# Kernel tuning notes

Measured on AMD Instinct MI355X. Metric: run time of the kernel, lower is better.

The kernel has to match this reference:

```python
import jax, jax.numpy as jnp
import numpy as np

# Mamba3TextEncoder config (class .small() defaults)
B_SZ, SEQ = 4, 512
VOCAB, D_MODEL, N_LAYERS = 32000, 768, 12
N_STATE, EXPAND, HEADDIM, NGROUPS, EMBED = 64, 2, 32, 1, 1536
D_INNER = EXPAND * D_MODEL            # 1536
NHEADS = D_INNER // HEADDIM           # 48
CONV_DIM = D_INNER + 2 * NGROUPS * N_STATE  # 1664 (x, B, C go through depthwise conv)
K_CONV = 4
PROJ_IN = 2 * D_INNER + 2 * NGROUPS * N_STATE + NHEADS  # z, xBC, dt


def setup_inputs() -> dict:
    key = jax.random.key(0)
    ks = jax.random.split(key, 16)
    s = 0.02
    return {
        "token_ids": jax.random.randint(ks[0], (B_SZ, SEQ), 0, VOCAB),
        "embed_W": jax.random.normal(ks[1], (VOCAB, D_MODEL), jnp.float32) * s,
        "ln_W": jnp.ones((N_LAYERS, D_MODEL), jnp.float32),
        "in_proj_W": jax.random.normal(ks[2], (N_LAYERS, D_MODEL, PROJ_IN), jnp.float32) * s,
        "conv_W": jax.random.normal(ks[3], (N_LAYERS, CONV_DIM, 1, K_CONV), jnp.float32) * 0.1,
        "conv_b": jnp.zeros((N_LAYERS, CONV_DIM), jnp.float32),
        "dt_bias": jax.random.uniform(ks[4], (N_LAYERS, NHEADS), jnp.float32, -4.6, -2.0),
        "A_log": jnp.tile(jnp.log(jnp.arange(1, NHEADS + 1, dtype=jnp.float32))[None], (N_LAYERS, 1)),
        "D": jnp.ones((N_LAYERS, NHEADS), jnp.float32),
        "norm_W": jnp.ones((N_LAYERS, D_INNER), jnp.float32),
        "out_proj_W": jax.random.normal(ks[5], (N_LAYERS, D_INNER, D_MODEL), jnp.float32) * s,
        "final_norm_W": jnp.ones((D_MODEL,), jnp.float32),
        "proj_W": jax.random.normal(ks[6], (D_MODEL, EMBED), jnp.float32) * s,
        "proj_b": jnp.zeros((EMBED,), jnp.float32),
    }


def _rmsnorm(x, w, eps=1e-5):
    return x * jax.lax.rsqrt(jnp.mean(x * x, axis=-1, keepdims=True) + eps) * w


def _causal_conv(x, w, b):
    # x: [B,S,C] depthwise causal conv, kernel K_CONV
    y = jax.lax.conv_general_dilated(
        x.transpose(0, 2, 1), w, (1,), [(K_CONV - 1, 0)],
        dimension_numbers=("NCH", "OIH", "NCH"), feature_group_count=CONV_DIM)
    return y.transpose(0, 2, 1) + b


def _ssm(xs, dt, A, Bm, Cm):
    # selective scan. xs:[B,S,H,P] dt:[B,S,H] A:[H] Bm,Cm:[B,S,N] (ngroups=1)
    decay = jnp.exp(dt * A)              # [B,S,H]
    dtx = dt[..., None] * xs             # [B,S,H,P]
    h0 = jnp.zeros((xs.shape[0], NHEADS, HEADDIM, N_STATE), xs.dtype)

    def step(h, inp):
        dec, dx, b, c = inp              # [B,H],[B,H,P],[B,N],[B,N]
        h = dec[..., None, None] * h + dx[..., None] * b[:, None, None, :]
        y = jnp.einsum("bhpn,bn->bhp", h, c)
        return h, y

    inputs = (decay.transpose(1, 0, 2), dtx.transpose(1, 0, 2, 3),
              Bm.transpose(1, 0, 2), Cm.transpose(1, 0, 2))
    _, ys = jax.lax.scan(step, h0, inputs)
    return ys.transpose(1, 0, 2, 3)      # [B,S,H,P]


def reference(token_ids, embed_W, ln_W, in_proj_W, conv_W, conv_b, dt_bias,
              A_log, D, norm_W, out_proj_W, final_norm_W, proj_W, proj_b):
    x = embed_W[token_ids]                               # [B,S,D]
    for l in range(N_LAYERS):
        h = _rmsnorm(x, ln_W[l])
        zxbcdt = h @ in_proj_W[l]                        # [B,S,PROJ_IN]
        z = zxbcdt[..., :D_INNER]
        xBC = zxbcdt[..., D_INNER:D_INNER + CONV_DIM]
        dt_raw = zxbcdt[..., D_INNER + CONV_DIM:]        # [B,S,H]
        xBC = jax.nn.silu(_causal_conv(xBC, conv_W[l], conv_b[l]))
        xs = xBC[..., :D_INNER].reshape(*xBC.shape[:2], NHEADS, HEADDIM)
        Bm = xBC[..., D_INNER:D_INNER + N_STATE]
        Cm = xBC[..., D_INNER + N_STATE:]
        dt = jax.nn.softplus(dt_raw + dt_bias[l])
        A = -jnp.exp(A_log[l])
        y = _ssm(xs, dt, A, Bm, Cm) + D[l][None, None, :, None] * xs
        y = y.reshape(*y.shape[:2], D_INNER)
        y = _rmsnorm(y * jax.nn.silu(z), norm_W[l])      # gated RMSNorm
        x = x + y @ out_proj_W[l]
    x = _rmsnorm(x, final_norm_W)
    pooled = x.mean(axis=1)                              # [B,D]
    proj = pooled @ proj_W + proj_b                      # [B,EMBED]
    n = jnp.sqrt(jnp.sum(proj * proj, axis=-1, keepdims=True))
    return proj / jnp.maximum(n, 1e-12)
```

## Files before the change

### kernel.cpp

```cpp
#include <hip/hip_runtime.h>
#include <math.h>

typedef __bf16 bf16x8 __attribute__((ext_vector_type(8)));
typedef short  s16x8  __attribute__((ext_vector_type(8)));
typedef float  f32x4  __attribute__((ext_vector_type(4)));

static constexpr int BSZ = 4, SEQ = 512, DM = 768;
static constexpr int DIN = 1536, NH = 48, HP = 32, NS = 64;
static constexpr int CDIM = 1664;
static constexpr int PROJ_IN = 3248;
static constexpr int LDZX = 3328;
static constexpr int ROWS = BSZ * SEQ;
static constexpr int EMBED = 1536;
static constexpr int NLAYERS = 12;

using gptr_t = const __attribute__((address_space(1))) void*;
using lptr_t = __attribute__((address_space(3))) void*;

__device__ __forceinline__ unsigned short f2bf(float f) {
  unsigned u = __builtin_bit_cast(unsigned, f);
  u += 0x7FFF + ((u >> 16) & 1);
  return (unsigned short)(u >> 16);
}
__device__ __forceinline__ float bf2f(unsigned short u) {
  unsigned v = (unsigned)u << 16;
  return __builtin_bit_cast(float, v);
}
__device__ __forceinline__ float sigm(float x) { return 1.f / (1.f + __expf(-x)); }
__device__ __forceinline__ float sp(float x) { return (x > 15.f) ? x : log1pf(__expf(x)); }

__device__ __forceinline__ void gll16(const void* g, void* l) {
  __builtin_amdgcn_global_load_lds((gptr_t)g, (lptr_t)l, 16, 0, 0);
}
__device__ __forceinline__ f32x4 mfma16(s16x8 a, s16x8 b, f32x4 c) {
  return __builtin_amdgcn_mfma_f32_16x16x32_bf16(
      __builtin_bit_cast(bf16x8, a), __builtin_bit_cast(bf16x8, b), c, 0, 0, 0);
}

template <int NW>
__device__ __forceinline__ float block_sum(float v) {
#pragma unroll
  for (int o = 32; o; o >>= 1) v += __shfl_xor(v, o);
  __shared__ float red[NW];
  if ((threadIdx.x & 63) == 0) red[threadIdx.x >> 6] = v;
  __syncthreads();
  float s = red[0];
#pragma unroll
  for (int i = 1; i < NW; ++i) s += red[i];
  return s;
}

__global__ void embed_k(const int* __restrict__ tok, const float* __restrict__ eW,
                        float* __restrict__ x, unsigned short* __restrict__ x16,
                        float* __restrict__ ssq1p) {
  int bt = blockIdx.x, tid = threadIdx.x;
  float4 v = ((const float4*)(eW + (size_t)tok[bt] * DM))[tid];
  ((float4*)(x + (size_t)bt * DM))[tid] = v;
  unsigned long long pk =
      (unsigned long long)f2bf(v.x) | ((unsigned long long)f2bf(v.y) << 16) |
      ((unsigned long long)f2bf(v.z) << 32) | ((unsigned long long)f2bf(v.w) << 48);
  *(unsigned long long*)(x16 + (size_t)bt * DM + tid * 4) = pk;
  float ss = v.x * v.x + v.y * v.y + v.z * v.z + v.w * v.w;
  float tot = block_sum<3>(ss);
  if (tid < 24) ssq1p[(size_t)bt * 24 + tid] = (tid == 0) ? tot : 0.f;
}

__global__ void transpose_cvt(const float* __restrict__ W, const float* __restrict__ sc,
                              unsigned short* __restrict__ Wt, int K, int N, int Npad) {
  __shared__ float tile[32][33];
  int l = blockIdx.z;
  const float* Wl = W + (size_t)l * K * N;
  const float* scl = sc + (size_t)l * K;
  unsigned short* Wtl = Wt + (size_t)l * Npad * K;
  int nb = blockIdx.x * 32, kb = blockIdx.y * 32;
  int tx = threadIdx.x, ty = threadIdx.y;
#pragma unroll
  for (int r = 0; r < 4; ++r) {
    int k = kb + ty + r * 8, n = nb + tx;
    tile[ty + r * 8][tx] = (n < N) ? Wl[(size_t)k * N + n] * scl[k] : 0.f;
  }
  __syncthreads();
#pragma unroll
  for (int r = 0; r < 4; ++r) {
    int n = nb + ty + r * 8, k = kb + tx;
    Wtl[(size_t)n * K + k] = f2bf(tile[tx][ty + r * 8]);
  }
}

template <int BM, int BN, int MODE>
__global__ __launch_bounds__(256) void gemm_k(
    const unsigned short* __restrict__ A, const unsigned short* __restrict__ Bt,
    int K, const float* __restrict__ ssqp, void* __restrict__ O0,
    void* __restrict__ O1, void* __restrict__ O2,
    unsigned short* __restrict__ x16o, float* __restrict__ ssqo) {
  constexpr int AIT = BM / 32, BIT = BN / 32, NST = AIT + BIT;
  constexpr int FM = BM / 32, FN = BN / 32;
  constexpr int NSSQ = (MODE == 0) ? 24 : 48;
  constexpr float INVD = (MODE == 0) ? (1.f / 768.f) : (1.f / 1536.f);
  __shared__ unsigned short lA[2][BM * 64], lB[2][BN * 64];
  __shared__ float rss[BM];
  int tid = threadIdx.x, lane = tid & 63, wv = tid >> 6;
  int flat = blockIdx.y * gridDim.x + blockIdx.x;
  int q8 = (gridDim.x * gridDim.y) >> 3;
  int nf = (flat & 7) * q8 + (flat >> 3);
  int bx = nf % gridDim.x, by = nf / gridDim.x;
  int m0 = by * BM, n0 = bx * BN;
  int wm = (wv >> 1) * (BM / 2), wn = (wv & 1) * (BN / 2);
  int NK = K >> 6;
  auto stage = [&](int kt, int buf) {
#pragma unroll
    for (int i = 0; i < AIT; ++i) {
      int flt = i * 256 + tid, rr = flt >> 3, cc = flt & 7;
      gll16(A + (size_t)(m0 + rr) * K + kt + (cc ^ (rr & 7)) * 8, (char*)lA[buf] + flt * 16);
    }
#pragma unroll
    for (int i = 0; i < BIT; ++i) {
      int flt = i * 256 + tid, rr = flt >> 3, cc = flt & 7;
      gll16(Bt + (size_t)(n0 + rr) * K + kt + (cc ^ (rr & 7)) * 8, (char*)lB[buf] + flt * 16);
    }
  };
  stage(0, 0);
  if (tid < BM) {
    const float* p = ssqp + (size_t)(m0 + tid) * NSSQ;
    float s = 0.f;
#pragma unroll
    for (int j = 0; j < NSSQ; ++j) s += p[j];
    rss[tid] = rsqrtf(s * INVD + 1e-5f);
  }
  __syncthreads();
  f32x4 acc[FM][FN] = {};
  for (int i = 0; i < NK; ++i) {
    if (i + 1 < NK) {
      stage((i + 1) << 6, (i + 1) & 1);
      asm volatile("s_waitcnt vmcnt(%0)" :: "i"(NST) : "memory");
    } else {
      asm volatile("s_waitcnt vmcnt(0)" ::: "memory");
    }
    __builtin_amdgcn_s_barrier();
    __builtin_amdgcn_sched_barrier(0);
    const unsigned short* cA = lA[i & 1];
    const unsigned short* cB = lB[i & 1];
#pragma unroll
    for (int ks = 0; ks < 2; ++ks) {
      s16x8 a[FM], b[FN];
#pragma unroll
      for (int mi = 0; mi < FM; ++mi) {
        int row = wm + mi * 16 + (lane & 15);
        int ch = (ks * 4 + (lane >> 4)) ^ (row & 7);
        a[mi] = *(const s16x8*)((const char*)cA + row * 128 + ch * 16);
      }
#pragma unroll
      for (int nj = 0; nj < FN; ++nj) {
        int row = wn + nj * 16 + (lane & 15);
        int ch = (ks * 4 + (lane >> 4)) ^ (row & 7);
        b[nj] = *(const s16x8*)((const char*)cB + row * 128 + ch * 16);
      }
#pragma unroll
      for (int mi = 0; mi < FM; ++mi)
#pragma unroll
        for (int nj = 0; nj < FN; ++nj)
          acc[mi][nj] = mfma16(a[mi], b[nj], acc[mi][nj]);
    }
    __builtin_amdgcn_s_barrier();
  }
#pragma unroll
  for (int mi = 0; mi < FM; ++mi) {
    int rl0 = wm + mi * 16 + ((lane >> 4) << 2);
    float rsr[4];
#pragma unroll
    for (int rg = 0; rg < 4; ++rg) rsr[rg] = rss[rl0 + rg];
    float part[4] = {0.f, 0.f, 0.f, 0.f};
#pragma unroll
    for (int nj = 0; nj < FN; ++nj) {
      int col = n0 + wn + nj * 16 + (lane & 15);
#pragma unroll
      for (int rg = 0; rg < 4; ++rg) {
        int row = m0 + rl0 + rg;
        float vv = acc[mi][nj][rg] * rsr[rg];
        if constexpr (MODE == 0) {
          if (n0 < DIN) {
            ((unsigned short*)O0)[(size_t)row * DIN + col] = f2bf(vv);
          } else if (n0 < DIN + CDIM) {
            ((float*)O1)[(size_t)row * CDIM + (col - DIN)] = vv;
          } else {
            int c2 = col - (DIN + CDIM);
            if (c2 < NH) ((float*)O2)[(size_t)row * NH + c2] = vv;
          }
        } else {
          size_t idx = (size_t)row * DM + col;
          float xn = vv + ((float*)O0)[idx];
          ((float*)O0)[idx] = xn;
          x16o[idx] = f2bf(xn);
          part[rg] += xn * xn;
        }
      }
    }
    if constexpr (MODE == 1) {
#pragma unroll
      for (int rg = 0; rg < 4; ++rg) {
#pragma unroll
        for (int off = 1; off < 16; off <<= 1) part[rg] += __shfl_xor(part[rg], off);
      }
      if ((lane & 15) == 0) {
#pragma unroll
        for (int rg = 0; rg < 4; ++rg)
          ssqo[(size_t)(m0 + rl0 + rg) * 24 + bx * 2 + (wn >> 5)] = part[rg];
      }
    }
  }
}

__global__ __launch_bounds__(256) void conv_dt_k(
    const float* __restrict__ xbc, const float* __restrict__ cw, const float* __restrict__ cb,
    const float* __restrict__ dtraw, const float* __restrict__ dbias,
    unsigned short* __restrict__ xs16, unsigned short* __restrict__ dtxT,
    unsigned short* __restrict__ Bbf, unsigned short* __restrict__ Cbf,
    float* __restrict__ dts) {
  __shared__ float stg[11][256];
  __shared__ float dtl[8][48];
  int tid = threadIdx.x;
  int chunk = blockIdx.x;
  int bt0 = blockIdx.y * 8;
  int t0 = bt0 & (SEQ - 1);
  int cbase = chunk * 256;
#pragma unroll
  for (int i = 0; i < 11; ++i) {
    int s = t0 - 3 + i, col = cbase + tid;
    stg[i][tid] = (s >= 0 && col < CDIM) ? xbc[(size_t)(bt0 - 3 + i) * CDIM + col] : 0.f;
  }
  if (chunk < 6) {
    for (int idx = tid; idx < 384; idx += 256) {
      int r = idx / 48, hh = idx - r * 48;
      dtl[r][hh] = sp(dtraw[(size_t)(bt0 + r) * NH + hh] + dbias[hh]);
    }
  }
  __syncthreads();
  int c = cbase + tid;
  if (chunk < 6) {
    float w0 = cw[c * 4], w1 = cw[c * 4 + 1], w2 = cw[c * 4 + 2], w3 = cw[c * 4 + 3];
    float bias = cb[c];
    int hh = c >> 5, p = c & 31, b = bt0 >> 9;
    s16x8 pk;
#pragma unroll
    for (int r = 0; r < 8; ++r) {
      float a = bias + stg[r][tid] * w0 + stg[r + 1][tid] * w1 + stg[r + 2][tid] * w2 +
                stg[r + 3][tid] * w3;
      float sv = a * sigm(a);
      xs16[(size_t)(bt0 + r) * DIN + c] = f2bf(sv);
      pk[r] = (short)f2bf(sv * dtl[r][hh]);
    }
    *reinterpret_cast<s16x8*>(dtxT + ((((size_t)b * NH + hh) * HP + p) * SEQ + t0)) = pk;
  } else if (tid < 128) {
    int cc = DIN + tid;
    float w0 = cw[cc * 4], w1 = cw[cc * 4 + 1], w2 = cw[cc * 4 + 2], w3 = cw[cc * 4 + 3];
    float bias = cb[cc];
#pragma unroll
    for (int r = 0; r < 8; ++r) {
      float a = bias + stg[r][tid] * w0 + stg[r + 1][tid] * w1 + stg[r + 2][tid] * w2 +
                stg[r + 3][tid] * w3;
      float sv = a * sigm(a);
      if (tid < 64) Bbf[(size_t)(bt0 + r) * NS + tid] = f2bf(sv);
      else          Cbf[(size_t)(bt0 + r) * NS + (tid - 64)] = f2bf(sv);
    }
  } else if (tid < 176) {
    int hh = tid - 128;
    float bias_ = dbias[hh];
    float v[8];
#pragma unroll
    for (int r = 0; r < 8; ++r) v[r] = sp(dtraw[(size_t)(bt0 + r) * NH + hh] + bias_);
    float4 a4 = {v[0], v[1], v[2], v[3]}, b4 = {v[4], v[5], v[6], v[7]};
    float* dp = dts + ((size_t)(bt0 >> 9) * NH + hh) * SEQ + t0;
    *(float4*)dp = a4;
    *(float4*)(dp + 4) = b4;
  }
}

__global__ __launch_bounds__(256) void scan_k(
    const unsigned short* __restrict__ Bbf, const unsigned short* __restrict__ Cbf,
    const unsigned short* __restrict__ dtxT, const unsigned short* __restrict__ xs16,
    const float* __restrict__ dts, const unsigned short* __restrict__ zb,
    const float* __restrict__ alog, const float* __restrict__ Dvec,
    unsigned short* __restrict__ g16, float* __restrict__ ssq2p) {
  __shared__ unsigned short CbPt[64 * 64];
  __shared__ unsigned short Bb[2][64 * 64], Dx[2][32 * 64];
  __shared__ float lsb[SEQ];
  __shared__ float pair[256];
  __shared__ int sfirst;
  int tid = threadIdx.x, lane = tid & 63, wv = tid >> 6;
  int tb = blockIdx.x, h = blockIdx.y, b = blockIdx.z;
  int t0 = tb * 64;
  const unsigned short* dxrow = dtxT + ((size_t)b * NH + h) * HP * SEQ;

#pragma unroll
  for (int i = 0; i < 2; ++i) {
    int flt = i * 256 + tid, rr = flt >> 3, cc = flt & 7;
    gll16(Cbf + (size_t)(b * SEQ + t0 + rr) * NS + (cc ^ (rr & 7)) * 8, (char*)CbPt + flt * 16);
  }
  float Ah = -__expf(alog[h]);
  int t2 = tid * 2;
  float2 dv = *(const float2*)(dts + ((size_t)b * NH + h) * SEQ + t2);
  float d0 = dv.x * Ah, d1 = dv.y * Ah;
  pair[tid] = d0 + d1;
  __syncthreads();
  for (int off = 1; off < 256; off <<= 1) {
    float add = (tid >= off) ? pair[tid - off] : 0.f;
    float cur = pair[tid];
    __syncthreads();
    pair[tid] = cur + add;
    __syncthreads();
  }
  float excl = tid ? pair[tid - 1] : 0.f;
  lsb[t2] = excl + d0;
  lsb[t2 + 1] = excl + d0 + d1;
  if (tid == 0) sfirst = tb;
  __syncthreads();
  float REF = lsb[t0];
  if (tid < tb && (REF - lsb[tid * 64 + 63] >= -12.f)) atomicMin(&sfirst, tid);
  __syncthreads();
  int st0 = sfirst;

#pragma unroll
  for (int i = 0; i < 2; ++i) {
    int flt = i * 256 + tid, rr = flt >> 3, cc = flt & 7;
    gll16(Bbf + (size_t)(b * SEQ + st0 * 64 + rr) * NS + (cc ^ (rr & 7)) * 8,
          (char*)Bb[st0 & 1] + flt * 16);
  }
  { int rr = tid >> 3, cc = tid & 7;
    gll16(dxrow + (size_t)rr * SEQ + st0 * 64 + (cc ^ (rr & 7)) * 8,
          (char*)Dx[st0 & 1] + tid * 16); }

  float lt[4], elt[4];
  int trb = wv * 16 + ((lane >> 4) << 2);
#pragma unroll
  for (int rg = 0; rg < 4; ++rg) {
    lt[rg] = lsb[t0 + trb + rg];
    elt[rg] = __expf(lt[rg] - REF);
  }
  s16x8 aC[2];
  f32x4 yacc[2] = {};

  for (int st = st0; st <= tb; ++st) {
    int s0 = st * 64;
    if (st < tb) {
      int s1 = s0 + 64;
#pragma unroll
      for (int i = 0; i < 2; ++i) {
        int flt = i * 256 + tid, rr = flt >> 3, cc = flt & 7;
        gll16(Bbf + (size_t)(b * SEQ + s1 + rr) * NS + (cc ^ (rr & 7)) * 8,
              (char*)Bb[(st + 1) & 1] + flt * 16);
      }
      { int rr = tid >> 3, cc = tid & 7;
        gll16(dxrow + (size_t)rr * SEQ + s1 + (cc ^ (rr & 7)) * 8,
              (char*)Dx[(st + 1) & 1] + tid * 16); }
      asm volatile("s_waitcnt vmcnt(3)" ::: "memory");
    } else {
      asm volatile("s_waitcnt vmcnt(0)" ::: "memory");
    }
    __builtin_amdgcn_s_barrier();
    __builtin_amdgcn_sched_barrier(0);
    const unsigned short* Bcur = Bb[st & 1];
    const unsigned short* Dcur = Dx[st & 1];
    if (st == st0) {
#pragma unroll
      for (int ks = 0; ks < 2; ++ks) {
        int row = wv * 16 + (lane & 15);
        int ch = (ks * 4 + (lane >> 4)) ^ (row & 7);
        aC[ks] = *(const s16x8*)((const char*)CbPt + row * 128 + ch * 16);
      }
    }
    float lsv[4];
#pragma unroll
    for (int sq = 0; sq < 4; ++sq) lsv[sq] = lsb[s0 + sq * 16 + (lane & 15)];
    f32x4 gf[4] = {};
#pragma unroll
    for (int sq = 0; sq < 4; ++sq)
#pragma unroll
      for (int ks = 0; ks < 2; ++ks) {
        int row = sq * 16 + (lane & 15);
        int ch = (ks * 4 + (lane >> 4)) ^ (row & 7);
        s16x8 bB = *(const s16x8*)((const char*)Bcur + row * 128 + ch * 16);
        gf[sq] = mfma16(aC[ks], bB, gf[sq]);
      }
    if (st < tb) {
      float es[4];
#pragma unroll
      for (int sq = 0; sq < 4; ++sq) es[sq] = __expf(REF - lsv[sq]);
#pragma unroll
      for (int sq = 0; sq < 4; ++sq) {
        int scol = sq * 16 + (lane & 15);
#pragma unroll
        for (int rg = 0; rg < 4; ++rg) {
          int trow = trb + rg;
          int off = (trow * 128 + scol * 2) ^ ((trow & 7) << 4);
          *(unsigned short*)((char*)CbPt + off) = f2bf(gf[sq][rg] * (elt[rg] * es[sq]));
        }
      }
    } else {
#pragma unroll
      for (int sq = 0; sq < 4; ++sq) {
        int scol = sq * 16 + (lane & 15);
        int sg = s0 + scol;
#pragma unroll
        for (int rg = 0; rg < 4; ++rg) {
          int trow = trb + rg, tg = t0 + trow;
          float wgt = (sg <= tg) ? __expf(lt[rg] - lsv[sq]) : 0.f;
          int off = (trow * 128 + scol * 2) ^ ((trow & 7) << 4);
          *(unsigned short*)((char*)CbPt + off) = f2bf(gf[sq][rg] * wgt);
        }
      }
    }
#pragma unroll
    for (int ks = 0; ks < 2; ++ks) {
      int row = wv * 16 + (lane & 15);
      int ch = (ks * 4 + (lane >> 4)) ^ (row & 7);
      s16x8 aP = *(const s16x8*)((const char*)CbPt + row * 128 + ch * 16);
#pragma unroll
      for (int pq = 0; pq < 2; ++pq) {
        int prow = pq * 16 + (lane & 15);
        int pch = (ks * 4 + (lane >> 4)) ^ (prow & 7);
        s16x8 bD = *(const s16x8*)((const char*)Dcur + prow * 128 + pch * 16);
        yacc[pq] = mfma16(aP, bD, yacc[pq]);
      }
    }
    __builtin_amdgcn_s_barrier();
  }
  float Dh = Dvec[h];
  float part[4] = {0.f, 0.f, 0.f, 0.f};
#pragma unroll
  for (int pq = 0; pq < 2; ++pq) {
#pragma unroll
    for (int rg = 0; rg < 4; ++rg) {
      int trow = trb + rg;
      int tg = t0 + trow;
      int p = pq * 16 + (lane & 15);
      size_t gi = (size_t)(b * SEQ + tg) * DIN + h * HP + p;
      float xv = bf2f(xs16[gi]);
      float yv = yacc[pq][rg] + Dh * xv;
      float zf = bf2f(zb[gi]);
      float g = yv * zf * sigm(zf);
      g16[gi] = f2bf(g);
      part[rg] += g * g;
    }
  }
#pragma unroll
  for (int rg = 0; rg < 4; ++rg) {
#pragma unroll
    for (int off = 1; off < 16; off <<= 1) part[rg] += __shfl_xor(part[rg], off);
  }
  if ((lane & 15) == 0) {
#pragma unroll
    for (int rg = 0; rg < 4; ++rg)
      ssq2p[(size_t)(b * SEQ + t0 + trb + rg) * 48 + h] = part[rg];
  }
}

__global__ void pool_k(const float* __restrict__ x, const float* __restrict__ ssq1p,
                       const float* __restrict__ fnW, float* __restrict__ pooled) {
  __shared__ float rsl[SEQ];
  int b = blockIdx.y, d0 = blockIdx.x * 256;
  for (int t = threadIdx.x; t < SEQ; t += 256) {
    const float* p = ssq1p + (size_t)(b * SEQ + t) * 24;
    float s = 0.f;
#pragma unroll
    for (int j = 0; j < 24; ++j) s += p[j];
    rsl[t] = rsqrtf(s * (1.f / DM) + 1e-5f);
  }
  __syncthreads();
  int d = d0 + threadIdx.x;
  float s = 0.f;
  for (int t = 0; t < SEQ; ++t) s += x[(size_t)(b * SEQ + t) * DM + d] * rsl[t];
  pooled[b * DM + d] = s * (1.f / SEQ) * fnW[d];
}
__global__ void proj_k(const float* __restrict__ pooled, const float* __restrict__ pW,
                       const float* __restrict__ pb, float* __restrict__ ptmp) {
  int e0 = blockIdx.x * 64, b = blockIdx.y;
  int el = threadIdx.x & 63, g = threadIdx.x >> 6;
  int e = e0 + el;
  float s = 0.f;
  for (int d = g * 192; d < (g + 1) * 192; ++d)
    s += pooled[b * DM + d] * pW[(size_t)d * EMBED + e];
  __shared__ float red[4][64];
  red[g][el] = s;
  __syncthreads();
  if (g == 0) ptmp[b * EMBED + e] = red[0][el] + red[1][el] + red[2][el] + red[3][el] + pb[e];
}
__global__ void l2_k(const float* __restrict__ ptmp, float* __restrict__ out) {
  int b = blockIdx.x;
  float v[6], ss = 0.f;
#pragma unroll
  for (int i = 0; i < 6; ++i) {
    v[i] = ptmp[(size_t)b * EMBED + threadIdx.x + i * 256];
    ss += v[i] * v[i];
  }
  float tot = block_sum<4>(ss);
  float inv = 1.f / fmaxf(sqrtf(tot), 1e-12f);
#pragma unroll
  for (int i = 0; i < 6; ++i)
    out[(size_t)b * EMBED + threadIdx.x + i * 256] = v[i] * inv;
}

extern "C" void kernel_launch(void* const* d_in, const int* in_sizes, int n_in,
                              void* d_out, int out_size, void* d_ws, size_t ws_size,
                              hipStream_t stream) {
  const int*   tok  = (const int*)d_in[0];
  const float* embW = (const float*)d_in[1];
  const float* lnW  = (const float*)d_in[2];
  const float* ipW  = (const float*)d_in[3];
  const float* cW   = (const float*)d_in[4];
  const float* cB   = (const float*)d_in[5];
  const float* dtB  = (const float*)d_in[6];
  const float* Alog = (const float*)d_in[7];
  const float* Dv   = (const float*)d_in[8];
  const float* nW   = (const float*)d_in[9];
  const float* opW  = (const float*)d_in[10];
  const float* fnW  = (const float*)d_in[11];
  const float* pW   = (const float*)d_in[12];
  const float* pb   = (const float*)d_in[13];
  float* out = (float*)d_out;

  char* wsp = (char*)d_ws;
  auto alloc = [&](size_t bytes) {
    char* p = wsp;
    wsp += (bytes + 255) & ~(size_t)255;
    return p;
  };
  float* x      = (float*)alloc((size_t)ROWS * DM * 4);
  float* xbc    = (float*)alloc((size_t)ROWS * CDIM * 4);
  float* dtraw  = (float*)alloc((size_t)ROWS * NH * 4);
  float* dts    = (float*)alloc((size_t)BSZ * NH * SEQ * 4);
  float* ssq1p  = (float*)alloc((size_t)ROWS * 24 * 4);
  float* ssq2p  = (float*)alloc((size_t)ROWS * 48 * 4);
  float* pooled = (float*)alloc((size_t)BSZ * DM * 4);
  float* ptmp   = (float*)alloc((size_t)BSZ * EMBED * 4);
  unsigned short* x16   = (unsigned short*)alloc((size_t)ROWS * DM * 2);
  unsigned short* zb    = (unsigned short*)alloc((size_t)ROWS * DIN * 2);
  unsigned short* xs16  = (unsigned short*)alloc((size_t)ROWS * DIN * 2);
  unsigned short* g16   = (unsigned short*)alloc((size_t)ROWS * DIN * 2);
  unsigned short* dtxT  = (unsigned short*)alloc((size_t)BSZ * NH * HP * SEQ * 2);
  unsigned short* Bbf   = (unsigned short*)alloc((size_t)ROWS * NS * 2);
  unsigned short* Cbf   = (unsigned short*)alloc((size_t)ROWS * NS * 2);
  unsigned short* wtA   = (unsigned short*)alloc((size_t)NLAYERS * LDZX * DM * 2);
  unsigned short* wtO   = (unsigned short*)alloc((size_t)NLAYERS * DM * DIN * 2);

  embed_k<<<ROWS, 192, 0, stream>>>(tok, embW, x, x16, ssq1p);
  transpose_cvt<<<dim3(LDZX / 32, DM / 32, NLAYERS), dim3(32, 8), 0, stream>>>(
      ipW, lnW, wtA, DM, PROJ_IN, LDZX);
  transpose_cvt<<<dim3(DM / 32, DIN / 32, NLAYERS), dim3(32, 8), 0, stream>>>(
      opW, nW, wtO, DIN, DM, DM);

  for (int l = 0; l < NLAYERS; ++l) {
    gemm_k<128, 128, 0><<<dim3(LDZX / 128, ROWS / 128), 256, 0, stream>>>(
        x16, wtA + (size_t)l * LDZX * DM, DM, ssq1p, zb, xbc, dtraw, nullptr, nullptr);
    conv_dt_k<<<dim3(7, ROWS / 8), 256, 0, stream>>>(
        xbc, cW + (size_t)l * CDIM * 4, cB + (size_t)l * CDIM, dtraw, dtB + l * NH,
        xs16, dtxT, Bbf, Cbf, dts);
    scan_k<<<dim3(SEQ / 64, NH, BSZ), 256, 0, stream>>>(
        Bbf, Cbf, dtxT, xs16, dts, zb, Alog + l * NH, Dv + l * NH, g16, ssq2p);
    gemm_k<64, 64, 1><<<dim3(DM / 64, ROWS / 64), 256, 0, stream>>>(
        g16, wtO + (size_t)l * DM * DIN, DIN, ssq2p, x, nullptr, nullptr, x16, ssq1p);
  }

  pool_k<<<dim3(DM / 256, BSZ), 256, 0, stream>>>(x, ssq1p, fnW, pooled);
  proj_k<<<dim3(EMBED / 64, BSZ), 256, 0, stream>>>(pooled, pW, pb, ptmp);
  l2_k<<<BSZ, 256, 0, stream>>>(ptmp, out);
}
```

Baseline: 950.0 us.

## Retile GEMMs to 2-wave blocks, vectorize transpose/conv loads, warp-shuffle scan prefix

The GEMM kernel is generalized over BK and warp count. Both projections now run with 2 waves per block, each wave covering full-width N tiles, and the out-projection uses BK=128. The row sum-of-squares partials shrink from 24 to 12 per row. The weight transpose and conv staging use float4 loads, the scan's block prefix sum switches from LDS barrier steps to wave shuffles, and s_setprio hints surround the MFMA sections. Together these aim to cut barrier and load-instruction overhead, at the cost of fewer waves per CU and higher register pressure per wave.

```diff
diff --git a/kernel.cpp b/kernel.cpp
--- a/kernel.cpp
+++ b/kernel.cpp
@@ -62,42 +62,62 @@
   *(unsigned long long*)(x16 + (size_t)bt * DM + tid * 4) = pk;
   float ss = v.x * v.x + v.y * v.y + v.z * v.z + v.w * v.w;
   float tot = block_sum<3>(ss);
-  if (tid < 24) ssq1p[(size_t)bt * 24 + tid] = (tid == 0) ? tot : 0.f;
+  if (tid < 12) ssq1p[(size_t)bt * 12 + tid] = (tid == 0) ? tot : 0.f;
 }
 
 __global__ void transpose_cvt(const float* __restrict__ W, const float* __restrict__ sc,
                               unsigned short* __restrict__ Wt, int K, int N, int Npad) {
-  __shared__ float tile[32][33];
+  __shared__ float tile[32][68];
   int l = blockIdx.z;
   const float* Wl = W + (size_t)l * K * N;
   const float* scl = sc + (size_t)l * K;
   unsigned short* Wtl = Wt + (size_t)l * Npad * K;
-  int nb = blockIdx.x * 32, kb = blockIdx.y * 32;
-  int tx = threadIdx.x, ty = threadIdx.y;
-#pragma unroll
-  for (int r = 0; r < 4; ++r) {
-    int k = kb + ty + r * 8, n = nb + tx;
-    tile[ty + r * 8][tx] = (n < N) ? Wl[(size_t)k * N + n] * scl[k] : 0.f;
-  }
-  __syncthreads();
-#pragma unroll
-  for (int r = 0; r < 4; ++r) {
-    int n = nb + ty + r * 8, k = kb + tx;
-    Wtl[(size_t)n * K + k] = f2bf(tile[tx][ty + r * 8]);
-  }
-}
-
-template <int BM, int BN, int MODE>
-__global__ __launch_bounds__(256) void gemm_k(
+  int nb = blockIdx.x * 64, kb = blockIdx.y * 32;
+  int tid = threadIdx.x;
+#pragma unroll
+  for (int rep = 0; rep < 2; ++rep) {
+    int f = rep * 256 + tid;
+    int k = f >> 4, c4 = f & 15;
+    int n = nb + c4 * 4;
+    float s = scl[kb + k];
+    float4 v = {0.f, 0.f, 0.f, 0.f};
+    if (n + 3 < N) {
+      v = *(const float4*)(Wl + (size_t)(kb + k) * N + n);
+    } else if (n < N) {
+      float t_[4] = {0.f, 0.f, 0.f, 0.f};
+      for (int j = 0; j < 4; ++j) if (n + j < N) t_[j] = Wl[(size_t)(kb + k) * N + n + j];
+      v = {t_[0], t_[1], t_[2], t_[3]};
+    }
+    tile[k][c4 * 4 + 0] = v.x * s; tile[k][c4 * 4 + 1] = v.y * s;
+    tile[k][c4 * 4 + 2] = v.z * s; tile[k][c4 * 4 + 3] = v.w * s;
+  }
+  __syncthreads();
+#pragma unroll
+  for (int rep = 0; rep < 2; ++rep) {
+    int f = rep * 256 + tid;
+    int n = f >> 3, k8 = f & 7;
+    unsigned long long pk =
+        (unsigned long long)f2bf(tile[k8 * 4 + 0][n]) |
+        ((unsigned long long)f2bf(tile[k8 * 4 + 1][n]) << 16) |
+        ((unsigned long long)f2bf(tile[k8 * 4 + 2][n]) << 32) |
+        ((unsigned long long)f2bf(tile[k8 * 4 + 3][n]) << 48);
+    *(unsigned long long*)(Wtl + (size_t)(nb + n) * K + kb + k8 * 4) = pk;
+  }
+}
+
+template <int BM, int BN, int BK, int NWARP, int MODE>
+__global__ __launch_bounds__(NWARP * 64) void gemm_k(
     const unsigned short* __restrict__ A, const unsigned short* __restrict__ Bt,
     int K, const float* __restrict__ ssqp, void* __restrict__ O0,
     void* __restrict__ O1, void* __restrict__ O2,
     unsigned short* __restrict__ x16o, float* __restrict__ ssqo) {
-  constexpr int AIT = BM / 32, BIT = BN / 32, NST = AIT + BIT;
-  constexpr int FM = BM / 32, FN = BN / 32;
-  constexpr int NSSQ = (MODE == 0) ? 24 : 48;
+  constexpr int THR = NWARP * 64;
+  constexpr int WROWS = BM / NWARP;
+  constexpr int FM = WROWS / 16, FN = BN / 16, KS = BK / 32, CH = BK / 8;
+  constexpr int AIT = (BM * CH) / THR, BIT = (BN * CH) / THR, NST = AIT + BIT;
+  constexpr int NSSQ = (MODE == 0) ? 12 : 48;
   constexpr float INVD = (MODE == 0) ? (1.f / 768.f) : (1.f / 1536.f);
-  __shared__ unsigned short lA[2][BM * 64], lB[2][BN * 64];
+  __shared__ unsigned short lA[2][BM * BK], lB[2][BN * BK];
   __shared__ float rss[BM];
   int tid = threadIdx.x, lane = tid & 63, wv = tid >> 6;
   int flat = blockIdx.y * gridDim.x + blockIdx.x;
@@ -105,18 +125,20 @@
   int nf = (flat & 7) * q8 + (flat >> 3);
   int bx = nf % gridDim.x, by = nf / gridDim.x;
   int m0 = by * BM, n0 = bx * BN;
-  int wm = (wv >> 1) * (BM / 2), wn = (wv & 1) * (BN / 2);
-  int NK = K >> 6;
+  int wm = wv * WROWS;
+  int NK = K / BK;
   auto stage = [&](int kt, int buf) {
 #pragma unroll
     for (int i = 0; i < AIT; ++i) {
-      int flt = i * 256 + tid, rr = flt >> 3, cc = flt & 7;
-      gll16(A + (size_t)(m0 + rr) * K + kt + (cc ^ (rr & 7)) * 8, (char*)lA[buf] + flt * 16);
+      int flt = i * THR + tid, rr = flt / CH, cc = flt % CH;
+      gll16(A + (size_t)(m0 + rr) * K + kt + ((cc ^ (rr & 7)) * 8),
+            (char*)lA[buf] + flt * 16);
     }
 #pragma unroll
     for (int i = 0; i < BIT; ++i) {
-      int flt = i * 256 + tid, rr = flt >> 3, cc = flt & 7;
-      gll16(Bt + (size_t)(n0 + rr) * K + kt + (cc ^ (rr & 7)) * 8, (char*)lB[buf] + flt * 16);
+      int flt = i * THR + tid, rr = flt / CH, cc = flt % CH;
+      gll16(Bt + (size_t)(n0 + rr) * K + kt + ((cc ^ (rr & 7)) * 8),
+            (char*)lB[buf] + flt * 16);
     }
   };
   stage(0, 0);
@@ -131,7 +153,7 @@
   f32x4 acc[FM][FN] = {};
   for (int i = 0; i < NK; ++i) {
     if (i + 1 < NK) {
-      stage((i + 1) << 6, (i + 1) & 1);
+      stage((i + 1) * BK, (i + 1) & 1);
       asm volatile("s_waitcnt vmcnt(%0)" :: "i"(NST) : "memory");
     } else {
       asm volatile("s_waitcnt vmcnt(0)" ::: "memory");
@@ -140,20 +162,21 @@
     __builtin_amdgcn_sched_barrier(0);
     const unsigned short* cA = lA[i & 1];
     const unsigned short* cB = lB[i & 1];
-#pragma unroll
-    for (int ks = 0; ks < 2; ++ks) {
+    __builtin_amdgcn_s_setprio(1);
+#pragma unroll
+    for (int ks = 0; ks < KS; ++ks) {
       s16x8 a[FM], b[FN];
 #pragma unroll
       for (int mi = 0; mi < FM; ++mi) {
         int row = wm + mi * 16 + (lane & 15);
         int ch = (ks * 4 + (lane >> 4)) ^ (row & 7);
-        a[mi] = *(const s16x8*)((const char*)cA + row * 128 + ch * 16);
+        a[mi] = *(const s16x8*)((const char*)cA + row * (CH * 16) + ch * 16);
       }
 #pragma unroll
       for (int nj = 0; nj < FN; ++nj) {
-        int row = wn + nj * 16 + (lane & 15);
+        int row = nj * 16 + (lane & 15);
         int ch = (ks * 4 + (lane >> 4)) ^ (row & 7);
-        b[nj] = *(const s16x8*)((const char*)cB + row * 128 + ch * 16);
+        b[nj] = *(const s16x8*)((const char*)cB + row * (CH * 16) + ch * 16);
       }
 #pragma unroll
       for (int mi = 0; mi < FM; ++mi)
@@ -161,6 +184,7 @@
         for (int nj = 0; nj < FN; ++nj)
           acc[mi][nj] = mfma16(a[mi], b[nj], acc[mi][nj]);
     }
+    __builtin_amdgcn_s_setprio(0);
     __builtin_amdgcn_s_barrier();
   }
 #pragma unroll
@@ -172,7 +196,7 @@
     float part[4] = {0.f, 0.f, 0.f, 0.f};
 #pragma unroll
     for (int nj = 0; nj < FN; ++nj) {
-      int col = n0 + wn + nj * 16 + (lane & 15);
+      int col = n0 + nj * 16 + (lane & 15);
 #pragma unroll
       for (int rg = 0; rg < 4; ++rg) {
         int row = m0 + rl0 + rg;
@@ -204,7 +228,7 @@
       if ((lane & 15) == 0) {
 #pragma unroll
         for (int rg = 0; rg < 4; ++rg)
-          ssqo[(size_t)(m0 + rl0 + rg) * 24 + bx * 2 + (wn >> 5)] = part[rg];
+          ssqo[(size_t)(m0 + rl0 + rg) * 12 + bx] = part[rg];
       }
     }
   }
@@ -223,10 +247,15 @@
   int bt0 = blockIdx.y * 8;
   int t0 = bt0 & (SEQ - 1);
   int cbase = chunk * 256;
-#pragma unroll
-  for (int i = 0; i < 11; ++i) {
-    int s = t0 - 3 + i, col = cbase + tid;
-    stg[i][tid] = (s >= 0 && col < CDIM) ? xbc[(size_t)(bt0 - 3 + i) * CDIM + col] : 0.f;
+  for (int f = tid; f < 11 * 64; f += 256) {
+    int row = f >> 6, c4 = f & 63;
+    int s = t0 - 3 + row;
+    int col = cbase + c4 * 4;
+    float4 v = {0.f, 0.f, 0.f, 0.f};
+    if (s >= 0 && col + 3 < CDIM) {
+      v = *(const float4*)(xbc + (size_t)(bt0 - 3 + row) * CDIM + col);
+    }
+    *(float4*)&stg[row][c4 * 4] = v;
   }
   if (chunk < 6) {
     for (int idx = tid; idx < 384; idx += 256) {
@@ -284,7 +313,7 @@
   __shared__ unsigned short CbPt[64 * 64];
   __shared__ unsigned short Bb[2][64 * 64], Dx[2][32 * 64];
   __shared__ float lsb[SEQ];
-  __shared__ float pair[256];
+  __shared__ float wtot[4];
   __shared__ int sfirst;
   int tid = threadIdx.x, lane = tid & 63, wv = tid >> 6;
   int tb = blockIdx.x, h = blockIdx.y, b = blockIdx.z;
@@ -300,19 +329,22 @@
   int t2 = tid * 2;
   float2 dv = *(const float2*)(dts + ((size_t)b * NH + h) * SEQ + t2);
   float d0 = dv.x * Ah, d1 = dv.y * Ah;
-  pair[tid] = d0 + d1;
-  __syncthreads();
-  for (int off = 1; off < 256; off <<= 1) {
-    float add = (tid >= off) ? pair[tid - off] : 0.f;
-    float cur = pair[tid];
-    __syncthreads();
-    pair[tid] = cur + add;
-    __syncthreads();
-  }
-  float excl = tid ? pair[tid - 1] : 0.f;
+  float ps = d0 + d1;
+  float v = ps;
+#pragma unroll
+  for (int off = 1; off < 64; off <<= 1) {
+    float u = __shfl_up(v, off);
+    if (lane >= off) v += u;
+  }
+  if (lane == 63) wtot[wv] = v;
+  if (tid == 0) sfirst = tb;
+  __syncthreads();
+  float wpre = 0.f;
+#pragma unroll
+  for (int w = 0; w < 3; ++w) wpre += (w < wv) ? wtot[w] : 0.f;
+  float excl = v + wpre - ps;
   lsb[t2] = excl + d0;
   lsb[t2 + 1] = excl + d0 + d1;
-  if (tid == 0) sfirst = tb;
   __syncthreads();
   float REF = lsb[t0];
   if (tid < tb && (REF - lsb[tid * 64 + 63] >= -12.f)) atomicMin(&sfirst, tid);
@@ -372,6 +404,7 @@
 #pragma unroll
     for (int sq = 0; sq < 4; ++sq) lsv[sq] = lsb[s0 + sq * 16 + (lane & 15)];
     f32x4 gf[4] = {};
+    __builtin_amdgcn_s_setprio(1);
 #pragma unroll
     for (int sq = 0; sq < 4; ++sq)
 #pragma unroll
@@ -381,6 +414,7 @@
         s16x8 bB = *(const s16x8*)((const char*)Bcur + row * 128 + ch * 16);
         gf[sq] = mfma16(aC[ks], bB, gf[sq]);
       }
+    __builtin_amdgcn_s_setprio(0);
     if (st < tb) {
       float es[4];
 #pragma unroll
@@ -409,6 +443,7 @@
         }
       }
     }
+    __builtin_amdgcn_s_setprio(1);
 #pragma unroll
     for (int ks = 0; ks < 2; ++ks) {
       int row = wv * 16 + (lane & 15);
@@ -422,6 +457,7 @@
         yacc[pq] = mfma16(aP, bD, yacc[pq]);
       }
     }
+    __builtin_amdgcn_s_setprio(0);
     __builtin_amdgcn_s_barrier();
   }
   float Dh = Dvec[h];
@@ -459,10 +495,10 @@
   __shared__ float rsl[SEQ];
   int b = blockIdx.y, d0 = blockIdx.x * 256;
   for (int t = threadIdx.x; t < SEQ; t += 256) {
-    const float* p = ssq1p + (size_t)(b * SEQ + t) * 24;
+    const float* p = ssq1p + (size_t)(b * SEQ + t) * 12;
     float s = 0.f;
 #pragma unroll
-    for (int j = 0; j < 24; ++j) s += p[j];
+    for (int j = 0; j < 12; ++j) s += p[j];
     rsl[t] = rsqrtf(s * (1.f / DM) + 1e-5f);
   }
   __syncthreads();
@@ -528,7 +564,7 @@
   float* xbc    = (float*)alloc((size_t)ROWS * CDIM * 4);
   float* dtraw  = (float*)alloc((size_t)ROWS * NH * 4);
   float* dts    = (float*)alloc((size_t)BSZ * NH * SEQ * 4);
-  float* ssq1p  = (float*)alloc((size_t)ROWS * 24 * 4);
+  float* ssq1p  = (float*)alloc((size_t)ROWS * 12 * 4);
   float* ssq2p  = (float*)alloc((size_t)ROWS * 48 * 4);
   float* pooled = (float*)alloc((size_t)BSZ * DM * 4);
   float* ptmp   = (float*)alloc((size_t)BSZ * EMBED * 4);
@@ -543,21 +579,21 @@
   unsigned short* wtO   = (unsigned short*)alloc((size_t)NLAYERS * DM * DIN * 2);
 
   embed_k<<<ROWS, 192, 0, stream>>>(tok, embW, x, x16, ssq1p);
-  transpose_cvt<<<dim3(LDZX / 32, DM / 32, NLAYERS), dim3(32, 8), 0, stream>>>(
+  transpose_cvt<<<dim3(LDZX / 64, DM / 32, NLAYERS), 256, 0, stream>>>(
       ipW, lnW, wtA, DM, PROJ_IN, LDZX);
-  transpose_cvt<<<dim3(DM / 32, DIN / 32, NLAYERS), dim3(32, 8), 0, stream>>>(
+  transpose_cvt<<<dim3(DM / 64, DIN / 32, NLAYERS), 256, 0, stream>>>(
       opW, nW, wtO, DIN, DM, DM);
 
   for (int l = 0; l < NLAYERS; ++l) {
-    gemm_k<128, 128, 0><<<dim3(LDZX / 128, ROWS / 128), 256, 0, stream>>>(
+    gemm_k<128, 128, 64, 2, 0><<<dim3(LDZX / 128, ROWS / 128), 128, 0, stream>>>(
         x16, wtA + (size_t)l * LDZX * DM, DM, ssq1p, zb, xbc, dtraw, nullptr, nullptr);
     conv_dt_k<<<dim3(7, ROWS / 8), 256, 0, stream>>>(
         xbc, cW + (size_t)l * CDIM * 4, cB + (size_t)l * CDIM, dtraw, dtB + l * NH,
         xs16, dtxT, Bbf, Cbf, dts);
     scan_k<<<dim3(SEQ / 64, NH, BSZ), 256, 0, stream>>>(
         Bbf, Cbf, dtxT, xs16, dts, zb, Alog + l * NH, Dv + l * NH, g16, ssq2p);
-    gemm_k<64, 64, 1><<<dim3(DM / 64, ROWS / 64), 256, 0, stream>>>(
-        g16, wtO + (size_t)l * DM * DIN, DIN, ssq2p, x, nullptr, nullptr, x16, ssq1p);
+    gemm_k<64, 64, 128, 2, 1><<<dim3(DM / 64, ROWS / 64), 128, 0, stream>>>(
+        g16, wtO + (size_t)l * DM * DIN, DIN, ssq2p, x, x, nullptr, x16, ssq1p);
   }
 
   pool_k<<<dim3(DM / 256, BSZ), 256, 0, stream>>>(x, ssq1p, fnW, pooled);
```

After: 1.111 ms. 17.0% more time.
